# Kernel optimization log

Hardware: AMD Instinct MI355X
Metric: run time of the kernel (lower is better)

The kernel has to match this reference:

```python
import jax, jax.numpy as jnp
import numpy as np

D_MODEL = 1024
NUM_HEADS = 16
D_HEAD = D_MODEL // NUM_HEADS
NEG_BIG = 10000000000.0  # matches the torch module's -1e10 mask constant


def setup_inputs() -> dict:
    key = jax.random.key(0)
    ks = jax.random.split(key, 9)
    d = D_MODEL
    scale = 1.0 / np.sqrt(d)
    inp = {
        "x": jax.random.normal(ks[0], (2, 2048, d), dtype=jnp.float32),
        "W_q": jax.random.normal(ks[1], (d, d), dtype=jnp.float32) * scale,
        "b_q": jnp.zeros((d,), dtype=jnp.float32),
        "W_k": jax.random.normal(ks[2], (d, d), dtype=jnp.float32) * scale,
        "b_k": jnp.zeros((d,), dtype=jnp.float32),
        "W_v": jax.random.normal(ks[3], (d, d), dtype=jnp.float32) * scale,
        "b_v": jnp.zeros((d,), dtype=jnp.float32),
        "W_o": jax.random.normal(ks[4], (d, d), dtype=jnp.float32) * scale,
        "b_o": jnp.zeros((d,), dtype=jnp.float32),
    }
    return inp


def reference(x, W_q, b_q, W_k, b_k, W_v, b_v, W_o, b_o):
    B, S, d = x.shape
    H, Dh = NUM_HEADS, D_HEAD

    Q = x @ W_q + b_q  # [B,S,d]
    K = x @ W_k + b_k
    V = x @ W_v + b_v

    # split heads: [B,S,d] -> [B,H,S,Dh]
    Qh = Q.reshape(B, S, H, Dh).transpose(0, 2, 1, 3)
    Kh = K.reshape(B, S, H, Dh).transpose(0, 2, 1, 3)
    Vh = V.reshape(B, S, H, Dh).transpose(0, 2, 1, 3)

    scores = jnp.einsum("bhid,bhjd->bhij", Qh, Kh) / jnp.sqrt(
        jnp.asarray(Dh, dtype=x.dtype)
    )

    # causal mask: tril(scores) - 1e10 * (1 - tril_mask)
    causal = jnp.tril(jnp.ones((S, S), dtype=x.dtype))
    scores = scores * causal - NEG_BIG * (1.0 - causal)

    attn = jax.nn.softmax(scores, axis=-1)  # dropout p=0.0 -> identity

    vals = jnp.einsum("bhij,bhjd->bhid", attn, Vh)  # [B,H,S,Dh]
    vals = vals.transpose(0, 2, 1, 3).reshape(B, S, d)

    return vals @ W_o + b_o
```

## Files before the change

### kernel.cpp

```cpp
#include <hip/hip_runtime.h>

typedef unsigned short u16;
typedef __attribute__((ext_vector_type(8))) short short8;
typedef __attribute__((ext_vector_type(4))) short shortx4;
typedef __attribute__((ext_vector_type(4))) float floatx4;

#define S_ 2048
#define D_ 1024
#define DQKV_ 3072
#define H_ 16
#define DH_ 64

#define EXP2F(x) __builtin_amdgcn_exp2f(x)

__device__ __forceinline__ float bf2f(u16 x) {
    union { unsigned int u; float f; } v; v.u = ((unsigned int)x) << 16; return v.f;
}
__device__ __forceinline__ u16 f2bf(float f) {
    unsigned int u = __float_as_uint(f);
    return (u16)((u + 0x7fffu + ((u >> 16) & 1u)) >> 16);
}
__device__ __forceinline__ u16 f2bf_fast(float f) {
    return (u16)((__float_as_uint(f) + 0x8000u) >> 16);
}

__device__ __forceinline__ void async16(const void* g, void* l) {
    __builtin_amdgcn_global_load_lds(
        (const __attribute__((address_space(1))) unsigned int*)g,
        (__attribute__((address_space(3))) unsigned int*)l, 16, 0, 0);
}

__global__ __launch_bounds__(256) void convert_x(const float* __restrict__ x, u16* __restrict__ xb) {
    const size_t i = ((size_t)blockIdx.x * 256 + threadIdx.x) * 4;
    float4 v = *(const float4*)&x[i];
    shortx4 h;
    h[0] = (short)f2bf(v.x); h[1] = (short)f2bf(v.y);
    h[2] = (short)f2bf(v.z); h[3] = (short)f2bf(v.w);
    *(shortx4*)&xb[i] = h;
}

__global__ __launch_bounds__(256) void transpose_w4(const float* __restrict__ Wq, const float* __restrict__ Wk,
                                                    const float* __restrict__ Wv, const float* __restrict__ Wo,
                                                    u16* __restrict__ Wqkvt, u16* __restrict__ Wot) {
    __shared__ u16 tile[32][33];
    const int z = blockIdx.z;
    const float* W = (z == 0) ? Wq : (z == 1) ? Wk : (z == 2) ? Wv : Wo;
    u16* dst = (z == 3) ? Wot : (Wqkvt + (size_t)z * D_ * D_);
    const int tx = threadIdx.x, ty = threadIdx.y;
    const int n0 = blockIdx.x * 32, k0 = blockIdx.y * 32;
#pragma unroll
    for (int r = 0; r < 4; ++r) {
        int k = ty + r * 8;
        tile[k][tx] = f2bf(W[(size_t)(k0 + k) * D_ + n0 + tx]);
    }
    __syncthreads();
#pragma unroll
    for (int r = 0; r < 4; ++r) {
        int n = ty + r * 8;
        dst[(size_t)(n0 + n) * D_ + k0 + tx] = tile[tx][n];
    }
}

__global__ __launch_bounds__(256) void transpose_headV(const u16* __restrict__ QKV, u16* __restrict__ Vt) {
    __shared__ u16 tile[64 * 65];
    const int t = threadIdx.x;
    const int bh = blockIdx.y, b = bh >> 4, h = bh & 15;
    const int s0 = blockIdx.x << 6;
#pragma unroll
    for (int i = 0; i < 16; ++i) {
        int idx = t + (i << 8);
        int s = idx >> 6, d = idx & 63;
        tile[s * 65 + d] = QKV[(size_t)(b * S_ + s0 + s) * DQKV_ + 2048 + h * DH_ + d];
    }
    __syncthreads();
#pragma unroll
    for (int i = 0; i < 16; ++i) {
        int idx = t + (i << 8);
        int d = idx >> 6, s = idx & 63;
        Vt[((size_t)bh * DH_ + d) * S_ + s0 + s] = tile[s * 65 + d];
    }
}

template <int BM, int BN, bool OUTF32>
__global__ __launch_bounds__(256) void gemm_bt(const u16* __restrict__ A, const u16* __restrict__ Bt,
                                               const float* __restrict__ b0, const float* __restrict__ b1,
                                               const float* __restrict__ b2, void* __restrict__ Cp,
                                               int M, int N, int Kd) {
    constexpr int FI = BM / 32, FJ = BN / 32;
    __shared__ __align__(16) u16 As[2][BM * 32];
    __shared__ __align__(16) u16 Bs[2][BN * 32];
    const int t = threadIdx.x;
    const int m0 = blockIdx.y * BM, n0 = blockIdx.x * BN;
    const int w = t >> 6, lane = t & 63;
    const int lr = lane & 15, lg = lane >> 4;
    const int wm = (w >> 1) * (BM / 2), wn = (w & 1) * (BN / 2);
    const int srow = lane >> 2, scol = (lane & 3) << 3;
    floatx4 acc[FI][FJ] = {};

    auto stage = [&](int buf, int k0) {
#pragma unroll
        for (int c = 0; c < BM / 64; ++c) {
            int rbase = (w * (BM / 64) + c) * 16;
            async16(&A[(size_t)(m0 + rbase + srow) * Kd + k0 + scol], &As[buf][rbase * 32]);
        }
#pragma unroll
        for (int c = 0; c < BN / 64; ++c) {
            int rbase = (w * (BN / 64) + c) * 16;
            async16(&Bt[(size_t)(n0 + rbase + srow) * Kd + k0 + scol], &Bs[buf][rbase * 32]);
        }
    };

    stage(0, 0);
    const int nk = Kd / 32;
    for (int kk = 0; kk < nk; ++kk) {
        const int cur = kk & 1;
        __syncthreads();
        if (kk + 1 < nk) stage(cur ^ 1, (kk + 1) * 32);

        short8 af[FI], bfr[FJ];
#pragma unroll
        for (int i = 0; i < FI; ++i) af[i]  = *(const short8*)&As[cur][(wm + i * 16 + lr) * 32 + lg * 8];
#pragma unroll
        for (int j = 0; j < FJ; ++j) bfr[j] = *(const short8*)&Bs[cur][(wn + j * 16 + lr) * 32 + lg * 8];
#pragma unroll
        for (int i = 0; i < FI; ++i)
#pragma unroll
            for (int j = 0; j < FJ; ++j)
                acc[i][j] = __builtin_amdgcn_mfma_f32_16x16x32_bf16(af[i], bfr[j], acc[i][j], 0, 0, 0);
    }

#pragma unroll
    for (int j = 0; j < FJ; ++j) {
        int col = n0 + wn + j * 16 + lr;
        const float* bp = (col < 1024) ? b0 : (col < 2048) ? b1 : b2;
        float bv = bp[col & 1023];
#pragma unroll
        for (int i = 0; i < FI; ++i) {
            int rb = m0 + wm + i * 16 + lg * 4;
#pragma unroll
            for (int ii = 0; ii < 4; ++ii) {
                float val = acc[i][j][ii] + bv;
                if (OUTF32) ((float*)Cp)[(size_t)(rb + ii) * N + col] = val;
                else        ((u16*)Cp)[(size_t)(rb + ii) * N + col] = f2bf(val);
            }
        }
    }
}

__global__ __launch_bounds__(256) void attn_mfma(const u16* __restrict__ QKV, const u16* __restrict__ Vt,
                                                 u16* __restrict__ O) {
    __shared__ __align__(16) u16 KsA[2][64 * 64];
    __shared__ __align__(16) u16 VsA[2][64 * 64];
    __shared__ __align__(16) u16 Ps[4 * 16 * 64];
    const int t = threadIdx.x, w = t >> 6, lane = t & 63;
    const int lr = lane & 15, lg = lane >> 4;
    const int bh = blockIdx.x, b = bh >> 4, h = bh & 15;
    const int qt = 31 - blockIdx.y;
    const int q0 = qt << 6;
    const float cs = 0.18033688f;

    const u16* Kb  = QKV + (size_t)b * S_ * DQKV_ + 1024 + h * DH_;
    const u16* Vtb = Vt + (size_t)bh * DH_ * S_;
    u16* Pw = Ps + w * (16 * 64);

    const int rb = lane >> 3;
    const int cc = ((lane & 7) ^ rb) << 3;
    const int swz = lr & 7;

    short8 qf[2];
#pragma unroll
    for (int ks = 0; ks < 2; ++ks)
        qf[ks] = *(const short8*)&QKV[(size_t)(b * S_ + q0 + w * 16 + lr) * DQKV_ + h * DH_ + ks * 32 + lg * 8];

    floatx4 of[4] = {};
    float lsum[4] = {0.f, 0.f, 0.f, 0.f};

    {
        u16* Kd = &KsA[0][w * 512];
        u16* Vd = &VsA[0][w * 512];
        async16(&Kb[(size_t)(w * 8 + rb) * DQKV_ + cc], Kd);
        async16(&Kb[(size_t)(32 + w * 8 + rb) * DQKV_ + cc], Kd + 2048);
        async16(&Vtb[(size_t)(w * 8 + rb) * S_ + cc], Vd);
        async16(&Vtb[(size_t)(32 + w * 8 + rb) * S_ + cc], Vd + 2048);
    }

    for (int kb = 0; kb <= qt; ++kb) {
        const int cur = kb & 1;
        __syncthreads();
        if (kb < qt) {
            const int K1 = (kb + 1) << 6;
            u16* Kd = &KsA[cur ^ 1][w * 512];
            u16* Vd = &VsA[cur ^ 1][w * 512];
            async16(&Kb[(size_t)(K1 + w * 8 + rb) * DQKV_ + cc], Kd);
            async16(&Kb[(size_t)(K1 + 32 + w * 8 + rb) * DQKV_ + cc], Kd + 2048);
            async16(&Vtb[(size_t)(w * 8 + rb) * S_ + K1 + cc], Vd);
            async16(&Vtb[(size_t)(32 + w * 8 + rb) * S_ + K1 + cc], Vd + 2048);
        }
        const u16* Kc = KsA[cur];
        const u16* Vc = VsA[cur];

        floatx4 sf[4] = {};
#pragma unroll
        for (int ks = 0; ks < 2; ++ks)
#pragma unroll
            for (int j = 0; j < 4; ++j) {
                short8 kf = *(const short8*)&Kc[(j * 16 + lr) * 64 + ((((ks << 2) + lg) ^ swz) << 3)];
                sf[j] = __builtin_amdgcn_mfma_f32_16x16x32_bf16(qf[ks], kf, sf[j], 0, 0, 0);
            }

        const bool diag = (kb == qt);
#pragma unroll
        for (int j = 0; j < 4; ++j)
#pragma unroll
            for (int ii = 0; ii < 4; ++ii) {
                float ev = EXP2F(sf[j][ii] * cs);
                if (diag && (j * 16 + lr > w * 16 + lg * 4 + ii)) ev = 0.f;
                lsum[ii] += ev;
                int r = lg * 4 + ii;
                int chunk = ((j * 2 + (lr >> 3)) ^ (r & 7));
                Pw[r * 64 + (chunk << 3) + (lr & 7)] = f2bf_fast(ev);
            }

#pragma unroll
        for (int ks = 0; ks < 2; ++ks) {
            short8 pa = *(const short8*)&Pw[lr * 64 + ((((ks << 2) + lg) ^ swz) << 3)];
#pragma unroll
            for (int j = 0; j < 4; ++j) {
                short8 vf = *(const short8*)&Vc[(j * 16 + lr) * 64 + ((((ks << 2) + lg) ^ swz) << 3)];
                of[j] = __builtin_amdgcn_mfma_f32_16x16x32_bf16(pa, vf, of[j], 0, 0, 0);
            }
        }
    }

    float rinv[4];
#pragma unroll
    for (int ii = 0; ii < 4; ++ii) {
        float s = lsum[ii];
#pragma unroll
        for (int off = 1; off < 16; off <<= 1) s += __shfl_xor(s, off);
        rinv[ii] = 1.f / s;
    }
#pragma unroll
    for (int j = 0; j < 4; ++j)
#pragma unroll
        for (int ii = 0; ii < 4; ++ii)
            O[(size_t)(b * S_ + q0 + w * 16 + lg * 4 + ii) * D_ + h * DH_ + j * 16 + lr] =
                f2bf(of[j][ii] * rinv[ii]);
}

extern "C" void kernel_launch(void* const* d_in, const int* in_sizes, int n_in,
                              void* d_out, int out_size, void* d_ws, size_t ws_size,
                              hipStream_t stream) {
    (void)in_sizes; (void)n_in; (void)out_size; (void)ws_size;
    const float* x  = (const float*)d_in[0];
    const float* Wq = (const float*)d_in[1];
    const float* bq = (const float*)d_in[2];
    const float* Wk = (const float*)d_in[3];
    const float* bk = (const float*)d_in[4];
    const float* Wv = (const float*)d_in[5];
    const float* bv = (const float*)d_in[6];
    const float* Wo = (const float*)d_in[7];
    const float* bo = (const float*)d_in[8];

    u16* ws    = (u16*)d_ws;
    u16* WqkvT = ws;
    u16* WoT   = ws + (size_t)3 * (1 << 20);
    u16* QKV   = ws + (size_t)4 * (1 << 20);
    u16* Vtm   = ws + (size_t)16 * (1 << 20);
    u16* xbf   = ws + (size_t)20 * (1 << 20);
    u16* Am    = ws + (size_t)20 * (1 << 20);

    convert_x<<<4096, 256, 0, stream>>>(x, xbf);
    transpose_w4<<<dim3(32, 32, 4), dim3(32, 8), 0, stream>>>(Wq, Wk, Wv, Wo, WqkvT, WoT);

    gemm_bt<128, 128, false><<<dim3(DQKV_ / 128, 4096 / 128), 256, 0, stream>>>(
        xbf, WqkvT, bq, bk, bv, QKV, 4096, DQKV_, 1024);

    transpose_headV<<<dim3(32, 32), 256, 0, stream>>>(QKV, Vtm);

    attn_mfma<<<dim3(32, 32), 256, 0, stream>>>(QKV, Vtm, Am);

    gemm_bt<64, 128, true><<<dim3(1024 / 128, 4096 / 64), 256, 0, stream>>>(
        Am, WoT, bo, bo, bo, d_out, 4096, 1024, 1024);
}
```

Measured before the change: 192.8 us.

## Restructure attention to 2 waves each owning 32 query rows with packed P stores

The attention kernel now runs 128 threads (2 waves) per block, and each wave processes two 16-row query fragments. This reuses every K and V fragment read from LDS for two MFMAs and halves the per-block staging and barrier overhead. P is converted with v_cvt_pk_bf16_f32 and stored as 8-byte packed writes, which needs a matching key permutation in the V transpose kernel. The diagonal mask is split into a compile-time specialised final iteration, and query tiles are issued in a snake order to balance the causal work. The trade-off is more registers per wave and fewer waves per block, so latency hiding relies on the two-blocks-per-CU launch bound.

```diff
diff --git a/kernel.cpp b/kernel.cpp
--- a/kernel.cpp
+++ b/kernel.cpp
@@ -4,6 +4,7 @@
 typedef __attribute__((ext_vector_type(8))) short short8;
 typedef __attribute__((ext_vector_type(4))) short shortx4;
 typedef __attribute__((ext_vector_type(4))) float floatx4;
+typedef __attribute__((ext_vector_type(2))) unsigned int uint2v;
 
 #define S_ 2048
 #define D_ 1024
@@ -13,6 +14,8 @@
 
 #define EXP2F(x) __builtin_amdgcn_exp2f(x)
 
+template <bool B> struct BoolC { static constexpr bool value = B; };
+
 __device__ __forceinline__ float bf2f(u16 x) {
     union { unsigned int u; float f; } v; v.u = ((unsigned int)x) << 16; return v.f;
 }
@@ -20,8 +23,10 @@
     unsigned int u = __float_as_uint(f);
     return (u16)((u + 0x7fffu + ((u >> 16) & 1u)) >> 16);
 }
-__device__ __forceinline__ u16 f2bf_fast(float f) {
-    return (u16)((__float_as_uint(f) + 0x8000u) >> 16);
+__device__ __forceinline__ unsigned int cvtpk_bf16(float lo, float hi) {
+    unsigned int r;
+    asm("v_cvt_pk_bf16_f32 %0, %1, %2" : "=v"(r) : "v"(lo), "v"(hi));
+    return r;
 }
 
 __device__ __forceinline__ void async16(const void* g, void* l) {
@@ -76,8 +81,9 @@
 #pragma unroll
     for (int i = 0; i < 16; ++i) {
         int idx = t + (i << 8);
-        int d = idx >> 6, s = idx & 63;
-        Vt[((size_t)bh * DH_ + d) * S_ + s0 + s] = tile[s * 65 + d];
+        int d = idx >> 6, p = idx & 63;
+        int sk = (p >> 2) | ((p & 3) << 4);
+        Vt[((size_t)bh * DH_ + d) * S_ + s0 + p] = tile[sk * 65 + d];
     }
 }
 
@@ -147,105 +153,121 @@
     }
 }
 
-__global__ __launch_bounds__(256) void attn_mfma(const u16* __restrict__ QKV, const u16* __restrict__ Vt,
-                                                 u16* __restrict__ O) {
+__global__ __launch_bounds__(128, 2) void attn_mfma(const u16* __restrict__ QKV, const u16* __restrict__ Vt,
+                                                    u16* __restrict__ O) {
     __shared__ __align__(16) u16 KsA[2][64 * 64];
     __shared__ __align__(16) u16 VsA[2][64 * 64];
-    __shared__ __align__(16) u16 Ps[4 * 16 * 64];
+    __shared__ __align__(16) u16 Ps[2 * 32 * 64];
     const int t = threadIdx.x, w = t >> 6, lane = t & 63;
     const int lr = lane & 15, lg = lane >> 4;
     const int bh = blockIdx.x, b = bh >> 4, h = bh & 15;
-    const int qt = 31 - blockIdx.y;
+    const int yy = blockIdx.y, uq = yy >> 3, aq = yy & 7;
+    const int qt = (uq << 3) | ((uq & 1) ? (7 - aq) : aq);
     const int q0 = qt << 6;
     const float cs = 0.18033688f;
 
     const u16* Kb  = QKV + (size_t)b * S_ * DQKV_ + 1024 + h * DH_;
     const u16* Vtb = Vt + (size_t)bh * DH_ * S_;
-    u16* Pw = Ps + w * (16 * 64);
+    u16* Pw = Ps + w * 2048;
 
     const int rb = lane >> 3;
     const int cc = ((lane & 7) ^ rb) << 3;
     const int swz = lr & 7;
 
-    short8 qf[2];
-#pragma unroll
-    for (int ks = 0; ks < 2; ++ks)
-        qf[ks] = *(const short8*)&QKV[(size_t)(b * S_ + q0 + w * 16 + lr) * DQKV_ + h * DH_ + ks * 32 + lg * 8];
-
-    floatx4 of[4] = {};
-    float lsum[4] = {0.f, 0.f, 0.f, 0.f};
-
-    {
-        u16* Kd = &KsA[0][w * 512];
-        u16* Vd = &VsA[0][w * 512];
-        async16(&Kb[(size_t)(w * 8 + rb) * DQKV_ + cc], Kd);
-        async16(&Kb[(size_t)(32 + w * 8 + rb) * DQKV_ + cc], Kd + 2048);
-        async16(&Vtb[(size_t)(w * 8 + rb) * S_ + cc], Vd);
-        async16(&Vtb[(size_t)(32 + w * 8 + rb) * S_ + cc], Vd + 2048);
-    }
-
-    for (int kb = 0; kb <= qt; ++kb) {
+    short8 qf[2][2];
+#pragma unroll
+    for (int m = 0; m < 2; ++m)
+#pragma unroll
+        for (int ks = 0; ks < 2; ++ks)
+            qf[m][ks] = *(const short8*)&QKV[(size_t)(b * S_ + q0 + w * 32 + m * 16 + lr) * DQKV_ +
+                                             h * DH_ + ks * 32 + lg * 8];
+
+    floatx4 of[2][4] = {};
+    float lsum[2][4] = {};
+
+    auto stage = [&](int buf, int kbase) {
+        u16* Kd = &KsA[buf][w * 2048];
+        u16* Vd = &VsA[buf][w * 2048];
+#pragma unroll
+        for (int c = 0; c < 4; ++c) {
+            async16(&Kb[(size_t)(kbase + w * 32 + c * 8 + rb) * DQKV_ + cc], Kd + c * 512);
+            async16(&Vtb[(size_t)(w * 32 + c * 8 + rb) * S_ + kbase + cc], Vd + c * 512);
+        }
+    };
+
+    stage(0, 0);
+
+    auto body = [&](int kb, auto diagc) {
+        constexpr bool DIAG = decltype(diagc)::value;
         const int cur = kb & 1;
         __syncthreads();
-        if (kb < qt) {
-            const int K1 = (kb + 1) << 6;
-            u16* Kd = &KsA[cur ^ 1][w * 512];
-            u16* Vd = &VsA[cur ^ 1][w * 512];
-            async16(&Kb[(size_t)(K1 + w * 8 + rb) * DQKV_ + cc], Kd);
-            async16(&Kb[(size_t)(K1 + 32 + w * 8 + rb) * DQKV_ + cc], Kd + 2048);
-            async16(&Vtb[(size_t)(w * 8 + rb) * S_ + K1 + cc], Vd);
-            async16(&Vtb[(size_t)(32 + w * 8 + rb) * S_ + K1 + cc], Vd + 2048);
-        }
+        if (kb < qt) stage(cur ^ 1, (kb + 1) << 6);
         const u16* Kc = KsA[cur];
         const u16* Vc = VsA[cur];
 
-        floatx4 sf[4] = {};
+        floatx4 sf[2][4] = {};
 #pragma unroll
         for (int ks = 0; ks < 2; ++ks)
 #pragma unroll
             for (int j = 0; j < 4; ++j) {
                 short8 kf = *(const short8*)&Kc[(j * 16 + lr) * 64 + ((((ks << 2) + lg) ^ swz) << 3)];
-                sf[j] = __builtin_amdgcn_mfma_f32_16x16x32_bf16(qf[ks], kf, sf[j], 0, 0, 0);
+                sf[0][j] = __builtin_amdgcn_mfma_f32_16x16x32_bf16(qf[0][ks], kf, sf[0][j], 0, 0, 0);
+                sf[1][j] = __builtin_amdgcn_mfma_f32_16x16x32_bf16(qf[1][ks], kf, sf[1][j], 0, 0, 0);
             }
 
-        const bool diag = (kb == qt);
-#pragma unroll
-        for (int j = 0; j < 4; ++j)
+#pragma unroll
+        for (int m = 0; m < 2; ++m)
 #pragma unroll
             for (int ii = 0; ii < 4; ++ii) {
-                float ev = EXP2F(sf[j][ii] * cs);
-                if (diag && (j * 16 + lr > w * 16 + lg * 4 + ii)) ev = 0.f;
-                lsum[ii] += ev;
-                int r = lg * 4 + ii;
-                int chunk = ((j * 2 + (lr >> 3)) ^ (r & 7));
-                Pw[r * 64 + (chunk << 3) + (lr & 7)] = f2bf_fast(ev);
+                const int r = lg * 4 + ii;
+                float ev[4];
+#pragma unroll
+                for (int j = 0; j < 4; ++j) {
+                    float e = EXP2F(sf[m][j][ii] * cs);
+                    if (DIAG && (j * 16 + lr > w * 32 + m * 16 + r)) e = 0.f;
+                    ev[j] = e;
+                }
+                lsum[m][ii] += (ev[0] + ev[1]) + (ev[2] + ev[3]);
+                uint2v pk;
+                pk.x = cvtpk_bf16(ev[0], ev[1]);
+                pk.y = cvtpk_bf16(ev[2], ev[3]);
+                *(uint2v*)&Pw[m * 1024 + r * 64 + ((((lr >> 1) ^ (r & 7)) << 3) | ((lr & 1) << 2))] = pk;
             }
 
 #pragma unroll
         for (int ks = 0; ks < 2; ++ks) {
-            short8 pa = *(const short8*)&Pw[lr * 64 + ((((ks << 2) + lg) ^ swz) << 3)];
+            short8 pa0 = *(const short8*)&Pw[lr * 64 + ((((ks << 2) + lg) ^ swz) << 3)];
+            short8 pa1 = *(const short8*)&Pw[1024 + lr * 64 + ((((ks << 2) + lg) ^ swz) << 3)];
 #pragma unroll
             for (int j = 0; j < 4; ++j) {
                 short8 vf = *(const short8*)&Vc[(j * 16 + lr) * 64 + ((((ks << 2) + lg) ^ swz) << 3)];
-                of[j] = __builtin_amdgcn_mfma_f32_16x16x32_bf16(pa, vf, of[j], 0, 0, 0);
+                of[0][j] = __builtin_amdgcn_mfma_f32_16x16x32_bf16(pa0, vf, of[0][j], 0, 0, 0);
+                of[1][j] = __builtin_amdgcn_mfma_f32_16x16x32_bf16(pa1, vf, of[1][j], 0, 0, 0);
             }
         }
-    }
-
-    float rinv[4];
-#pragma unroll
-    for (int ii = 0; ii < 4; ++ii) {
-        float s = lsum[ii];
-#pragma unroll
-        for (int off = 1; off < 16; off <<= 1) s += __shfl_xor(s, off);
-        rinv[ii] = 1.f / s;
-    }
-#pragma unroll
-    for (int j = 0; j < 4; ++j)
-#pragma unroll
-        for (int ii = 0; ii < 4; ++ii)
-            O[(size_t)(b * S_ + q0 + w * 16 + lg * 4 + ii) * D_ + h * DH_ + j * 16 + lr] =
-                f2bf(of[j][ii] * rinv[ii]);
+    };
+
+    for (int kb = 0; kb < qt; ++kb) body(kb, BoolC<false>{});
+    body(qt, BoolC<true>{});
+
+    float rinv[2][4];
+#pragma unroll
+    for (int m = 0; m < 2; ++m)
+#pragma unroll
+        for (int ii = 0; ii < 4; ++ii) {
+            float s = lsum[m][ii];
+#pragma unroll
+            for (int off = 1; off < 16; off <<= 1) s += __shfl_xor(s, off);
+            rinv[m][ii] = 1.f / s;
+        }
+#pragma unroll
+    for (int m = 0; m < 2; ++m)
+#pragma unroll
+        for (int j = 0; j < 4; ++j)
+#pragma unroll
+            for (int ii = 0; ii < 4; ++ii)
+                O[(size_t)(b * S_ + q0 + w * 32 + m * 16 + lg * 4 + ii) * D_ + h * DH_ + j * 16 + lr] =
+                    f2bf(of[m][j][ii] * rinv[m][ii]);
 }
 
 extern "C" void kernel_launch(void* const* d_in, const int* in_sizes, int n_in,
@@ -278,7 +300,7 @@
 
     transpose_headV<<<dim3(32, 32), 256, 0, stream>>>(QKV, Vtm);
 
-    attn_mfma<<<dim3(32, 32), 256, 0, stream>>>(QKV, Vtm, Am);
+    attn_mfma<<<dim3(32, 32), 128, 0, stream>>>(QKV, Vtm, Am);
 
     gemm_bt<64, 128, true><<<dim3(1024 / 128, 4096 / 64), 256, 0, stream>>>(
         Am, WoT, bo, bo, bo, d_out, 4096, 1024, 1024);
```

Measured after the change: 200.5 us. 1.04x slower.

## Keep softmax probabilities in registers by computing transposed scores and permuting V

Applied to the files above, without the earlier changes.

The attention kernel now computes S^T (K as the A operand), so each lane holds probabilities laid out as the A-fragment for the PV MFMA. That removes the per-wave LDS round trip for P. The V transpose kernel permutes key positions to match the new register layout, P is packed with v_cvt_pk_bf16_f32, and the diagonal block is peeled so the mask check is compiled out of the main loop. Row sums now need a cross-lane shuffle at the end, and correctness depends on the permutation matching the MFMA fragment layout exactly.

```diff
diff --git a/kernel.cpp b/kernel.cpp
--- a/kernel.cpp
+++ b/kernel.cpp
@@ -13,6 +13,8 @@
 
 #define EXP2F(x) __builtin_amdgcn_exp2f(x)
 
+template <bool B> struct BoolC { static constexpr bool value = B; };
+
 __device__ __forceinline__ float bf2f(u16 x) {
     union { unsigned int u; float f; } v; v.u = ((unsigned int)x) << 16; return v.f;
 }
@@ -20,8 +22,10 @@
     unsigned int u = __float_as_uint(f);
     return (u16)((u + 0x7fffu + ((u >> 16) & 1u)) >> 16);
 }
-__device__ __forceinline__ u16 f2bf_fast(float f) {
-    return (u16)((__float_as_uint(f) + 0x8000u) >> 16);
+__device__ __forceinline__ unsigned int cvtpk_bf16(float lo, float hi) {
+    unsigned int r;
+    asm("v_cvt_pk_bf16_f32 %0, %1, %2" : "=v"(r) : "v"(lo), "v"(hi));
+    return r;
 }
 
 __device__ __forceinline__ void async16(const void* g, void* l) {
@@ -76,8 +80,9 @@
 #pragma unroll
     for (int i = 0; i < 16; ++i) {
         int idx = t + (i << 8);
-        int d = idx >> 6, s = idx & 63;
-        Vt[((size_t)bh * DH_ + d) * S_ + s0 + s] = tile[s * 65 + d];
+        int d = idx >> 6, p = idx & 63;
+        int sk = ((p >> 5) << 5) | (((p >> 2) & 1) << 4) | (((p >> 3) & 3) << 2) | (p & 3);
+        Vt[((size_t)bh * DH_ + d) * S_ + s0 + p] = tile[sk * 65 + d];
     }
 }
 
@@ -151,7 +156,6 @@
                                                  u16* __restrict__ O) {
     __shared__ __align__(16) u16 KsA[2][64 * 64];
     __shared__ __align__(16) u16 VsA[2][64 * 64];
-    __shared__ __align__(16) u16 Ps[4 * 16 * 64];
     const int t = threadIdx.x, w = t >> 6, lane = t & 63;
     const int lr = lane & 15, lg = lane >> 4;
     const int bh = blockIdx.x, b = bh >> 4, h = bh & 15;
@@ -161,7 +165,6 @@
 
     const u16* Kb  = QKV + (size_t)b * S_ * DQKV_ + 1024 + h * DH_;
     const u16* Vtb = Vt + (size_t)bh * DH_ * S_;
-    u16* Pw = Ps + w * (16 * 64);
 
     const int rb = lane >> 3;
     const int cc = ((lane & 7) ^ rb) << 3;
@@ -173,29 +176,24 @@
         qf[ks] = *(const short8*)&QKV[(size_t)(b * S_ + q0 + w * 16 + lr) * DQKV_ + h * DH_ + ks * 32 + lg * 8];
 
     floatx4 of[4] = {};
-    float lsum[4] = {0.f, 0.f, 0.f, 0.f};
-
-    {
-        u16* Kd = &KsA[0][w * 512];
-        u16* Vd = &VsA[0][w * 512];
-        async16(&Kb[(size_t)(w * 8 + rb) * DQKV_ + cc], Kd);
-        async16(&Kb[(size_t)(32 + w * 8 + rb) * DQKV_ + cc], Kd + 2048);
-        async16(&Vtb[(size_t)(w * 8 + rb) * S_ + cc], Vd);
-        async16(&Vtb[(size_t)(32 + w * 8 + rb) * S_ + cc], Vd + 2048);
-    }
-
-    for (int kb = 0; kb <= qt; ++kb) {
+    float lsum = 0.f;
+
+    auto stage = [&](int buf, int kbase) {
+        u16* Kd = &KsA[buf][w * 512];
+        u16* Vd = &VsA[buf][w * 512];
+        async16(&Kb[(size_t)(kbase + w * 8 + rb) * DQKV_ + cc], Kd);
+        async16(&Kb[(size_t)(kbase + 32 + w * 8 + rb) * DQKV_ + cc], Kd + 2048);
+        async16(&Vtb[(size_t)(w * 8 + rb) * S_ + kbase + cc], Vd);
+        async16(&Vtb[(size_t)(32 + w * 8 + rb) * S_ + kbase + cc], Vd + 2048);
+    };
+
+    stage(0, 0);
+
+    auto body = [&](int kb, auto diagc) {
+        constexpr bool DIAG = decltype(diagc)::value;
         const int cur = kb & 1;
         __syncthreads();
-        if (kb < qt) {
-            const int K1 = (kb + 1) << 6;
-            u16* Kd = &KsA[cur ^ 1][w * 512];
-            u16* Vd = &VsA[cur ^ 1][w * 512];
-            async16(&Kb[(size_t)(K1 + w * 8 + rb) * DQKV_ + cc], Kd);
-            async16(&Kb[(size_t)(K1 + 32 + w * 8 + rb) * DQKV_ + cc], Kd + 2048);
-            async16(&Vtb[(size_t)(w * 8 + rb) * S_ + K1 + cc], Vd);
-            async16(&Vtb[(size_t)(32 + w * 8 + rb) * S_ + K1 + cc], Vd + 2048);
-        }
+        if (kb < qt) stage(cur ^ 1, (kb + 1) << 6);
         const u16* Kc = KsA[cur];
         const u16* Vc = VsA[cur];
 
@@ -203,49 +201,57 @@
 #pragma unroll
         for (int ks = 0; ks < 2; ++ks)
 #pragma unroll
-            for (int j = 0; j < 4; ++j) {
-                short8 kf = *(const short8*)&Kc[(j * 16 + lr) * 64 + ((((ks << 2) + lg) ^ swz) << 3)];
-                sf[j] = __builtin_amdgcn_mfma_f32_16x16x32_bf16(qf[ks], kf, sf[j], 0, 0, 0);
-            }
-
-        const bool diag = (kb == qt);
-#pragma unroll
-        for (int j = 0; j < 4; ++j)
+            for (int tt = 0; tt < 4; ++tt) {
+                short8 kf = *(const short8*)&Kc[(tt * 16 + lr) * 64 + ((((ks << 2) + lg) ^ swz) << 3)];
+                sf[tt] = __builtin_amdgcn_mfma_f32_16x16x32_bf16(kf, qf[ks], sf[tt], 0, 0, 0);
+            }
+
+        float ev[4][4];
+#pragma unroll
+        for (int tt = 0; tt < 4; ++tt) {
+            float s0;
 #pragma unroll
             for (int ii = 0; ii < 4; ++ii) {
-                float ev = EXP2F(sf[j][ii] * cs);
-                if (diag && (j * 16 + lr > w * 16 + lg * 4 + ii)) ev = 0.f;
-                lsum[ii] += ev;
-                int r = lg * 4 + ii;
-                int chunk = ((j * 2 + (lr >> 3)) ^ (r & 7));
-                Pw[r * 64 + (chunk << 3) + (lr & 7)] = f2bf_fast(ev);
-            }
+                float e = EXP2F(sf[tt][ii] * cs);
+                if (DIAG && (tt * 16 + lg * 4 + ii > w * 16 + lr)) e = 0.f;
+                ev[tt][ii] = e;
+                s0 = (ii == 0) ? e : s0 + e;
+            }
+            lsum += s0;
+        }
 
 #pragma unroll
         for (int ks = 0; ks < 2; ++ks) {
-            short8 pa = *(const short8*)&Pw[lr * 64 + ((((ks << 2) + lg) ^ swz) << 3)];
-#pragma unroll
-            for (int j = 0; j < 4; ++j) {
-                short8 vf = *(const short8*)&Vc[(j * 16 + lr) * 64 + ((((ks << 2) + lg) ^ swz) << 3)];
-                of[j] = __builtin_amdgcn_mfma_f32_16x16x32_bf16(pa, vf, of[j], 0, 0, 0);
-            }
-        }
-    }
-
-    float rinv[4];
-#pragma unroll
-    for (int ii = 0; ii < 4; ++ii) {
-        float s = lsum[ii];
-#pragma unroll
-        for (int off = 1; off < 16; off <<= 1) s += __shfl_xor(s, off);
-        rinv[ii] = 1.f / s;
-    }
-#pragma unroll
-    for (int j = 0; j < 4; ++j)
+            union { short8 s; unsigned int u[4]; } pk;
+            pk.u[0] = cvtpk_bf16(ev[2 * ks][0], ev[2 * ks][1]);
+            pk.u[1] = cvtpk_bf16(ev[2 * ks][2], ev[2 * ks][3]);
+            pk.u[2] = cvtpk_bf16(ev[2 * ks + 1][0], ev[2 * ks + 1][1]);
+            pk.u[3] = cvtpk_bf16(ev[2 * ks + 1][2], ev[2 * ks + 1][3]);
+#pragma unroll
+            for (int tt = 0; tt < 4; ++tt) {
+                short8 vf = *(const short8*)&Vc[(tt * 16 + lr) * 64 + ((((ks << 2) + lg) ^ swz) << 3)];
+                of[tt] = __builtin_amdgcn_mfma_f32_16x16x32_bf16(pk.s, vf, of[tt], 0, 0, 0);
+            }
+        }
+    };
+
+    for (int kb = 0; kb < qt; ++kb) body(kb, BoolC<false>{});
+    body(qt, BoolC<true>{});
+
+    lsum += __shfl_xor(lsum, 16);
+    lsum += __shfl_xor(lsum, 32);
+    const float rinv = 1.f / lsum;
+    float rv[4];
+#pragma unroll
+    for (int ii = 0; ii < 4; ++ii)
+        rv[ii] = __shfl(rinv, (lane & 48) | (lg * 4 + ii));
+
+#pragma unroll
+    for (int tt = 0; tt < 4; ++tt)
 #pragma unroll
         for (int ii = 0; ii < 4; ++ii)
-            O[(size_t)(b * S_ + q0 + w * 16 + lg * 4 + ii) * D_ + h * DH_ + j * 16 + lr] =
-                f2bf(of[j][ii] * rinv[ii]);
+            O[(size_t)(b * S_ + q0 + w * 16 + lg * 4 + ii) * D_ + h * DH_ + tt * 16 + lr] =
+                f2bf(of[tt][ii] * rv[ii]);
 }
 
 extern "C" void kernel_launch(void* const* d_in, const int* in_sizes, int n_in,
```

Result: no change. 191.1 us (-0.9%).
